# Kernel tuning notes

Measured on AMD Instinct MI355X. Metric: run time of the kernel, lower is better.

The kernel has to match this reference:

```python
import jax, jax.numpy as jnp
import numpy as np

B, N, D, H = 8, 1024, 1024, 16
DH = D // H
SCALE = DH ** -0.5
NEG = -1e9


def setup_inputs() -> dict:
    key = jax.random.key(0)
    k1, k2, k3, k4 = jax.random.split(key, 4)
    x = jax.random.normal(k1, (B, N, D), dtype=jnp.float32)
    mask = jax.random.randint(k2, (B, N), 0, 2, dtype=jnp.int32)
    w_qkv = jax.random.normal(k3, (D, 3 * D), dtype=jnp.float32) * (D ** -0.5)
    w_out = jax.random.normal(k4, (D, D), dtype=jnp.float32) * (D ** -0.5)
    b_out = jnp.zeros((D,), dtype=jnp.float32)
    return {"x": x, "mask": mask, "w_qkv": w_qkv, "w_out": w_out, "b_out": b_out}


def reference(x, mask, w_qkv, w_out, b_out):
    b, n, d = x.shape
    qkv = x @ w_qkv  # [b, n, 3d]
    q, k, v = jnp.split(qkv, 3, axis=-1)
    # [b, n, d] -> [b, h, n, dh]
    reshape = lambda t: t.reshape(b, n, H, DH).transpose(0, 2, 1, 3)
    q, k, v = reshape(q), reshape(k), reshape(v)
    dots = jnp.einsum("bhqd,bhkd->bhqk", q, k) * SCALE  # [b, h, n, n]
    # mask [b, n] -> [b, 1, n]; broadcasts over heads and query dim (masks keys)
    m = (mask == 0)[:, None, None, :]
    dots = jnp.where(m, NEG, dots)
    attn = jax.nn.softmax(dots, axis=-1)
    out = jnp.einsum("bhqk,bhkd->bhqd", attn, v)  # [b, h, n, dh]
    out = out.transpose(0, 2, 1, 3).reshape(b, n, d)  # [b, n, d]
    out = out @ w_out + b_out
    return out, attn
```

## Files before the change

kernel.cpp:

```cpp
#include <hip/hip_runtime.h>
#include <hip/hip_bf16.h>

typedef unsigned short u16;
typedef __attribute__((ext_vector_type(8))) short bf16x8;
typedef __attribute__((ext_vector_type(4))) float f32x4;

#define DEVI __device__ __forceinline__

constexpr float SCALE = 0.125f;

DEVI float bf2f(u16 u) { unsigned v = ((unsigned)u) << 16; float f; __builtin_memcpy(&f, &v, 4); return f; }
DEVI u16 f2bf(float f) { __hip_bfloat16 h = __float2bfloat16(f); u16 u; __builtin_memcpy(&u, &h, 2); return u; }

DEVI void gload_lds16(const u16* g, u16* l) {
    __builtin_amdgcn_global_load_lds(
        (const __attribute__((address_space(1))) unsigned int*)g,
        (__attribute__((address_space(3))) unsigned int*)l, 16, 0, 0);
}

__global__ __launch_bounds__(256) void cast_f32_bf16(const float* __restrict__ in,
                                                     u16* __restrict__ out, int n) {
    int i = (blockIdx.x * 256 + threadIdx.x) * 4;
    if (i >= n) return;
    float4 v = *(const float4*)(in + i);
    ushort4 o;
    o.x = f2bf(v.x); o.y = f2bf(v.y); o.z = f2bf(v.z); o.w = f2bf(v.w);
    *(ushort4*)(out + i) = o;
}

__global__ __launch_bounds__(256) void transpose_f32_bf16(const float* __restrict__ in,
                                                          u16* __restrict__ out,
                                                          int R, int C) {
    __shared__ u16 t[64][65];
    int r0 = blockIdx.y * 64, c0 = blockIdx.x * 64;
    int tid = threadIdx.x;
    for (int i = 0; i < 16; i++) {
        int idx = tid + i * 256; int r = idx >> 6, c = idx & 63;
        t[r][c] = f2bf(in[(size_t)(r0 + r) * C + c0 + c]);
    }
    __syncthreads();
    for (int i = 0; i < 16; i++) {
        int idx = tid + i * 256; int c = idx >> 6, r = idx & 63;
        out[(size_t)(c0 + c) * R + r0 + r] = t[r][c];
    }
}

__global__ __launch_bounds__(256) void make_vt(const u16* __restrict__ qkv,
                                               u16* __restrict__ vt) {
    __shared__ u16 t[64][65];
    int bh = blockIdx.y; int b = bh >> 4, h = bh & 15;
    int n0 = blockIdx.x * 64;
    int tid = threadIdx.x;
    const u16* src = qkv + (size_t)b * 1024 * 3072 + 2048 + h * 64;
    for (int i = 0; i < 16; i++) {
        int idx = tid + i * 256; int n = idx >> 6, d = idx & 63;
        t[n][d] = src[(size_t)(n0 + n) * 3072 + d];
    }
    __syncthreads();
    u16* dst = vt + (size_t)bh * 64 * 1024;
    for (int i = 0; i < 16; i++) {
        int idx = tid + i * 256; int d = idx >> 6, n = idx & 63;
        dst[(size_t)d * 1024 + n0 + n] = t[n][d];
    }
}

template <bool BIAS, bool F32OUT>
__global__ __launch_bounds__(256) void gemm_bt(const u16* __restrict__ A,
                                               const u16* __restrict__ Bt,
                                               const float* __restrict__ bias,
                                               void* __restrict__ Cv,
                                               int M, int N, int K) {
    __shared__ alignas(16) u16 As[128 * 64];
    __shared__ alignas(16) u16 Bs[128 * 64];
    int tid = threadIdx.x;
    int wave = tid >> 6, lane = tid & 63, quad = lane >> 4, lm = lane & 15;
    int bm = blockIdx.y * 128, bn = blockIdx.x * 128;
    int wm = (wave >> 1) * 64, wn = (wave & 1) * 64;

    f32x4 acc[4][4];
    for (int i = 0; i < 4; i++) for (int j = 0; j < 4; j++) acc[i][j] = f32x4{0.f, 0.f, 0.f, 0.f};

    int lrow8 = lane >> 3;
    int lcol  = (lane & 7) * 8;

    for (int kb = 0; kb < K; kb += 64) {
        for (int i = 0; i < 4; i++) {
            int c = wave * 4 + i;
            int row = c * 8 + lrow8;
            gload_lds16(A  + (size_t)(bm + row) * K + kb + lcol, &As[c * 512 + lane * 8]);
            gload_lds16(Bt + (size_t)(bn + row) * K + kb + lcol, &Bs[c * 512 + lane * 8]);
        }
        __syncthreads();
        for (int ks = 0; ks < 2; ks++) {
            bf16x8 af[4], bfr[4];
            for (int mt = 0; mt < 4; mt++)
                af[mt] = *(const bf16x8*)(&As[(wm + mt * 16 + lm) * 64 + ks * 32 + quad * 8]);
            for (int nt = 0; nt < 4; nt++)
                bfr[nt] = *(const bf16x8*)(&Bs[(wn + nt * 16 + lm) * 64 + ks * 32 + quad * 8]);
            for (int mt = 0; mt < 4; mt++)
                for (int nt = 0; nt < 4; nt++)
                    acc[mt][nt] = __builtin_amdgcn_mfma_f32_16x16x32_bf16(
                        af[mt], bfr[nt], acc[mt][nt], 0, 0, 0);
        }
        __syncthreads();
    }
    for (int mt = 0; mt < 4; mt++)
        for (int nt = 0; nt < 4; nt++) {
            int col = bn + wn + nt * 16 + lm;
            float bv = BIAS ? bias[col] : 0.f;
            for (int r = 0; r < 4; r++) {
                int row = bm + wm + mt * 16 + quad * 4 + r;
                if (F32OUT) ((float*)Cv)[(size_t)row * N + col] = acc[mt][nt][r] + bv;
                else        ((u16*)Cv)[(size_t)row * N + col] = f2bf(acc[mt][nt][r] + bv);
            }
        }
}

__global__ __launch_bounds__(256) void attn_mfma(const u16* __restrict__ qkv,
                                                 const u16* __restrict__ vt,
                                                 const int* __restrict__ mask,
                                                 float* __restrict__ attn_out,
                                                 u16* __restrict__ o_ws) {
    constexpr int LDT = 72;
    __shared__ alignas(16) u16 Ks[64 * LDT];
    __shared__ alignas(16) u16 Vs[64 * LDT];
    __shared__ alignas(16) u16 Ps[64 * LDT];

    int tid = threadIdx.x;
    int wave = tid >> 6, lane = tid & 63, quad = lane >> 4, lm = lane & 15;
    int bh = blockIdx.y; int b = bh >> 4, h = bh & 15;
    int qb = blockIdx.x;
    int qrow0 = qb * 64 + wave * 16;

    bf16x8 qf[2];
    {
        const u16* qptr = qkv + (size_t)(b * 1024 + qrow0 + lm) * 3072 + h * 64 + quad * 8;
        qf[0] = *(const bf16x8*)(qptr);
        qf[1] = *(const bf16x8*)(qptr + 32);
    }
    const u16* kbase  = qkv + (size_t)b * 1024 * 3072 + 1024 + h * 64;
    const u16* vtbase = vt + (size_t)bh * 64 * 1024;
    const int* mrow   = mask + b * 1024;

    float l_r[4] = {0.f, 0.f, 0.f, 0.f};
    for (int kb = 0; kb < 16; kb++) {
        for (int i = 0; i < 2; i++) {
            int c = tid + i * 256; int r = c >> 3, off = c & 7;
            *(bf16x8*)(&Ks[r * LDT + off * 8]) =
                *(const bf16x8*)(kbase + (size_t)(kb * 64 + r) * 3072 + off * 8);
        }
        __syncthreads();
        f32x4 acc[4];
        for (int nt = 0; nt < 4; nt++) acc[nt] = f32x4{0.f, 0.f, 0.f, 0.f};
        for (int ks = 0; ks < 2; ks++)
            for (int nt = 0; nt < 4; nt++) {
                bf16x8 kf = *(const bf16x8*)(&Ks[(nt * 16 + lm) * LDT + ks * 32 + quad * 8]);
                acc[nt] = __builtin_amdgcn_mfma_f32_16x16x32_bf16(qf[ks], kf, acc[nt], 0, 0, 0);
            }
        for (int nt = 0; nt < 4; nt++) {
            bool mk = (mrow[kb * 64 + nt * 16 + lm] != 0);
            for (int r = 0; r < 4; r++)
                l_r[r] += mk ? __expf(acc[nt][r] * SCALE) : 0.f;
        }
        __syncthreads();
    }
    float invl[4];
    for (int r = 0; r < 4; r++) {
        float l = l_r[r];
        for (int s = 8; s >= 1; s >>= 1) l += __shfl_xor(l, s, 64);
        invl[r] = 1.0f / l;
    }

    f32x4 oacc[4];
    for (int nt = 0; nt < 4; nt++) oacc[nt] = f32x4{0.f, 0.f, 0.f, 0.f};
    for (int kb = 0; kb < 16; kb++) {
        for (int i = 0; i < 2; i++) {
            int c = tid + i * 256; int r = c >> 3, off = c & 7;
            *(bf16x8*)(&Ks[r * LDT + off * 8]) =
                *(const bf16x8*)(kbase + (size_t)(kb * 64 + r) * 3072 + off * 8);
            *(bf16x8*)(&Vs[r * LDT + off * 8]) =
                *(const bf16x8*)(vtbase + (size_t)r * 1024 + kb * 64 + off * 8);
        }
        __syncthreads();
        f32x4 acc[4];
        for (int nt = 0; nt < 4; nt++) acc[nt] = f32x4{0.f, 0.f, 0.f, 0.f};
        for (int ks = 0; ks < 2; ks++)
            for (int nt = 0; nt < 4; nt++) {
                bf16x8 kf = *(const bf16x8*)(&Ks[(nt * 16 + lm) * LDT + ks * 32 + quad * 8]);
                acc[nt] = __builtin_amdgcn_mfma_f32_16x16x32_bf16(qf[ks], kf, acc[nt], 0, 0, 0);
            }
        for (int nt = 0; nt < 4; nt++) {
            bool mk = (mrow[kb * 64 + nt * 16 + lm] != 0);
            for (int r = 0; r < 4; r++) {
                float p = mk ? __expf(acc[nt][r] * SCALE) * invl[r] : 0.f;
                attn_out[((size_t)bh * 1024 + qb * 64 + wave * 16 + quad * 4 + r) * 1024
                         + kb * 64 + nt * 16 + lm] = p;
                Ps[(wave * 16 + quad * 4 + r) * LDT + nt * 16 + lm] = f2bf(p);
            }
        }
        __syncthreads();
        for (int ks = 0; ks < 2; ks++) {
            bf16x8 pf = *(const bf16x8*)(&Ps[(wave * 16 + lm) * LDT + ks * 32 + quad * 8]);
            for (int nt = 0; nt < 4; nt++) {
                bf16x8 vf = *(const bf16x8*)(&Vs[(nt * 16 + lm) * LDT + ks * 32 + quad * 8]);
                oacc[nt] = __builtin_amdgcn_mfma_f32_16x16x32_bf16(pf, vf, oacc[nt], 0, 0, 0);
            }
        }
        __syncthreads();
    }
    for (int nt = 0; nt < 4; nt++)
        for (int r = 0; r < 4; r++) {
            int row = qb * 64 + wave * 16 + quad * 4 + r;
            o_ws[(size_t)(b * 1024 + row) * 1024 + h * 64 + nt * 16 + lm] = f2bf(oacc[nt][r]);
        }
}

extern "C" void kernel_launch(void* const* d_in, const int* in_sizes, int n_in,
                              void* d_out, int out_size, void* d_ws, size_t ws_size,
                              hipStream_t stream) {
    const float* x    = (const float*)d_in[0];
    const int*   mask = (const int*)d_in[1];
    const float* wqkv = (const float*)d_in[2];
    const float* wout = (const float*)d_in[3];
    const float* bout = (const float*)d_in[4];

    float* out  = (float*)d_out;
    float* attn = out + (size_t)8192 * 1024;

    char* ws = (char*)d_ws;
    u16* xbf   = (u16*)(ws);
    u16* vt    = xbf;
    u16* qkv   = (u16*)(ws + 16777216);
    u16* o_ws  = (u16*)(ws + 67108864);
    u16* wqkvT = (u16*)(ws + 83886080);
    u16* woutT = (u16*)(ws + 90177536);

    cast_f32_bf16<<<dim3(8192), 256, 0, stream>>>(x, xbf, 8388608);
    transpose_f32_bf16<<<dim3(48, 16), 256, 0, stream>>>(wqkv, wqkvT, 1024, 3072);
    transpose_f32_bf16<<<dim3(16, 16), 256, 0, stream>>>(wout, woutT, 1024, 1024);
    gemm_bt<false, false><<<dim3(24, 64), 256, 0, stream>>>(xbf, wqkvT, nullptr, qkv, 8192, 3072, 1024);
    make_vt<<<dim3(16, 128), 256, 0, stream>>>(qkv, vt);
    attn_mfma<<<dim3(16, 128), 256, 0, stream>>>(qkv, vt, mask, attn, o_ws);
    gemm_bt<true, true><<<dim3(8, 64), 256, 0, stream>>>(o_ws, woutT, bout, out, 8192, 1024, 1024);
}
```

Measured before the change: 841.7 us.

## Load K/V fragments directly from global memory and swizzle block order for L2 locality

```diff
diff --git a/kernel.cpp b/kernel.cpp
--- a/kernel.cpp
+++ b/kernel.cpp
@@ -122,14 +122,15 @@
                                                  float* __restrict__ attn_out,
                                                  u16* __restrict__ o_ws) {
     constexpr int LDT = 72;
-    __shared__ alignas(16) u16 Ks[64 * LDT];
-    __shared__ alignas(16) u16 Vs[64 * LDT];
     __shared__ alignas(16) u16 Ps[64 * LDT];
 
     int tid = threadIdx.x;
     int wave = tid >> 6, lane = tid & 63, quad = lane >> 4, lm = lane & 15;
-    int bh = blockIdx.y; int b = bh >> 4, h = bh & 15;
-    int qb = blockIdx.x;
+
+    int flat = blockIdx.y * gridDim.x + blockIdx.x;
+    int swz = (flat & 7) * 256 + (flat >> 3);
+    int bh = swz >> 4, qb = swz & 15;
+    int b = bh >> 4, h = bh & 15;
     int qrow0 = qb * 64 + wave * 16;
 
     bf16x8 qf[2];
@@ -144,17 +145,12 @@
 
     float l_r[4] = {0.f, 0.f, 0.f, 0.f};
     for (int kb = 0; kb < 16; kb++) {
-        for (int i = 0; i < 2; i++) {
-            int c = tid + i * 256; int r = c >> 3, off = c & 7;
-            *(bf16x8*)(&Ks[r * LDT + off * 8]) =
-                *(const bf16x8*)(kbase + (size_t)(kb * 64 + r) * 3072 + off * 8);
-        }
-        __syncthreads();
         f32x4 acc[4];
         for (int nt = 0; nt < 4; nt++) acc[nt] = f32x4{0.f, 0.f, 0.f, 0.f};
         for (int ks = 0; ks < 2; ks++)
             for (int nt = 0; nt < 4; nt++) {
-                bf16x8 kf = *(const bf16x8*)(&Ks[(nt * 16 + lm) * LDT + ks * 32 + quad * 8]);
+                bf16x8 kf = *(const bf16x8*)(kbase +
+                    (size_t)(kb * 64 + nt * 16 + lm) * 3072 + ks * 32 + quad * 8);
                 acc[nt] = __builtin_amdgcn_mfma_f32_16x16x32_bf16(qf[ks], kf, acc[nt], 0, 0, 0);
             }
         for (int nt = 0; nt < 4; nt++) {
@@ -162,7 +158,6 @@
             for (int r = 0; r < 4; r++)
                 l_r[r] += mk ? __expf(acc[nt][r] * SCALE) : 0.f;
         }
-        __syncthreads();
     }
     float invl[4];
     for (int r = 0; r < 4; r++) {
@@ -174,19 +169,12 @@
     f32x4 oacc[4];
     for (int nt = 0; nt < 4; nt++) oacc[nt] = f32x4{0.f, 0.f, 0.f, 0.f};
     for (int kb = 0; kb < 16; kb++) {
-        for (int i = 0; i < 2; i++) {
-            int c = tid + i * 256; int r = c >> 3, off = c & 7;
-            *(bf16x8*)(&Ks[r * LDT + off * 8]) =
-                *(const bf16x8*)(kbase + (size_t)(kb * 64 + r) * 3072 + off * 8);
-            *(bf16x8*)(&Vs[r * LDT + off * 8]) =
-                *(const bf16x8*)(vtbase + (size_t)r * 1024 + kb * 64 + off * 8);
-        }
-        __syncthreads();
         f32x4 acc[4];
         for (int nt = 0; nt < 4; nt++) acc[nt] = f32x4{0.f, 0.f, 0.f, 0.f};
         for (int ks = 0; ks < 2; ks++)
             for (int nt = 0; nt < 4; nt++) {
-                bf16x8 kf = *(const bf16x8*)(&Ks[(nt * 16 + lm) * LDT + ks * 32 + quad * 8]);
+                bf16x8 kf = *(const bf16x8*)(kbase +
+                    (size_t)(kb * 64 + nt * 16 + lm) * 3072 + ks * 32 + quad * 8);
                 acc[nt] = __builtin_amdgcn_mfma_f32_16x16x32_bf16(qf[ks], kf, acc[nt], 0, 0, 0);
             }
         for (int nt = 0; nt < 4; nt++) {
@@ -198,15 +186,14 @@
                 Ps[(wave * 16 + quad * 4 + r) * LDT + nt * 16 + lm] = f2bf(p);
             }
         }
-        __syncthreads();
         for (int ks = 0; ks < 2; ks++) {
             bf16x8 pf = *(const bf16x8*)(&Ps[(wave * 16 + lm) * LDT + ks * 32 + quad * 8]);
             for (int nt = 0; nt < 4; nt++) {
-                bf16x8 vf = *(const bf16x8*)(&Vs[(nt * 16 + lm) * LDT + ks * 32 + quad * 8]);
+                bf16x8 vf = *(const bf16x8*)(vtbase +
+                    (size_t)(nt * 16 + lm) * 1024 + kb * 64 + ks * 32 + quad * 8);
                 oacc[nt] = __builtin_amdgcn_mfma_f32_16x16x32_bf16(pf, vf, oacc[nt], 0, 0, 0);
             }
         }
-        __syncthreads();
     }
     for (int nt = 0; nt < 4; nt++)
         for (int r = 0; r < 4; r++) {
```

Result: slower. 1.007 ms (+19.6%).
